# Performance work log

Hardware: AMD Instinct MI355X
Metric: run time of the kernel (lower is better)

## Reference

```python
import jax, jax.numpy as jnp
import numpy as np
import math

NUM_FREQ = 16           # pos_encoder octave frequencies
LATENT_SPACING = 3.0
PE_DIM = 4 * NUM_FREQ   # sin/cos for x and y


def pos_encode(delta_x, delta_y, physical_scale):
    # Fourier RPE: [..., 4*NUM_FREQ]
    freqs = (2.0 ** jnp.arange(NUM_FREQ, dtype=delta_x.dtype)) * jnp.pi
    ax = (delta_x / physical_scale)[..., None] * freqs  # [..., nf]
    ay = (delta_y / physical_scale)[..., None] * freqs
    return jnp.concatenate([jnp.sin(ax), jnp.cos(ax), jnp.sin(ay), jnp.cos(ay)], axis=-1)


def setup_inputs() -> dict:
    key = jax.random.key(0)
    B, L = 4, 4096
    positions = jax.random.normal(key, (B, L, 2), dtype=jnp.float32) * 50.0
    return {"positions": positions, "k": 16}


def reference(positions, k):
    B, L, _ = positions.shape
    k = min(k, L - 1)
    physical_scale = LATENT_SPACING * math.sqrt(k / math.pi)

    # full pairwise squared distances [B, L, L], diagonal masked to +inf
    diff_all = positions[:, :, None, :] - positions[:, None, :, :]
    dist_sq_all = jnp.sum(diff_all * diff_all, axis=-1)
    dist_sq_all = jnp.where(jnp.eye(L, dtype=bool)[None], jnp.inf, dist_sq_all)

    # smallest-k via top_k on negated distances
    _, topk_indices = jax.lax.top_k(-dist_sq_all, k)  # [B, L, k]

    # gather neighbor positions: [B, L, k, 2]
    neighbor_positions = jnp.take_along_axis(
        positions[:, None, :, :], topk_indices[..., None], axis=2)

    delta = neighbor_positions - positions[:, :, None, :]
    delta_x, delta_y = delta[..., 0], delta[..., 1]
    distances = jnp.sqrt(delta_x**2 + delta_y**2 + 1e-8)  # [B, L, k]

    rpe = pos_encode(delta_x, delta_y, physical_scale)  # [B, L, k, PE_DIM]

    zeros = jnp.zeros((B, L, 1), dtype=positions.dtype)
    self_rpe = pos_encode(zeros, zeros, physical_scale)  # [B, L, 1, PE_DIM]

    return topk_indices, rpe, self_rpe, distances, neighbor_positions
```

## Files before the change

kernel.cpp:

```cpp
#include <hip/hip_runtime.h>
#include <math.h>

namespace {
constexpr int BB  = 4;
constexpr int LL  = 4096;
constexpr int KK  = 16;
constexpr int GRID = 64;
constexpr int NCELL = GRID * GRID;
constexpr float WORLD_LO = -256.0f, CELL_INV = 0.125f;

constexpr int WSB_U32   = 6208;
constexpr int SIDX_OFF  = 4104;
constexpr int HARD_CNT  = BB * WSB_U32;
constexpr int HARD_LIST = HARD_CNT + 1;
constexpr int HARD_CAP  = 1024;

constexpr size_t N_IDX    = (size_t)BB * LL * KK;
constexpr size_t OFF_RPE  = N_IDX;
constexpr size_t OFF_SELF = OFF_RPE + N_IDX * 64;
constexpr size_t OFF_DIST = OFF_SELF + (size_t)BB * LL * 64;
constexpr size_t OFF_NPOS = OFF_DIST + N_IDX;
}

__device__ __forceinline__ float bf16r(float x) {
  unsigned u = __float_as_uint(x);
  unsigned r = (u + 0x7FFFu + ((u >> 16) & 1u)) & 0xFFFF0000u;
  return __uint_as_float(r);
}

__device__ __forceinline__ float d2_of(float cx, float cy, float px, float py) {
  const float dx = cx - px, dy = cy - py;
  return __fadd_rn(__fmul_rn(dx, dx), __fmul_rn(dy, dy));
}

__device__ __forceinline__ void insert16(unsigned long long (&key)[KK],
                                         unsigned long long kj) {
  #pragma unroll
  for (int t = 0; t < KK; ++t) {
    const bool lt = kj < key[t];
    const unsigned long long nk = lt ? kj : key[t];
    const unsigned long long ok = lt ? key[t] : kj;
    key[t] = nk; kj = ok;
  }
}

__device__ __forceinline__ int nth_set(unsigned long long m, int n) {
  int src = 0;
  #pragma unroll
  for (int w = 32; w >= 1; w >>= 1) {
    const unsigned long long lowm = (w == 64) ? ~0ull : ((1ull << w) - 1ull);
    const int c = __popcll(m & lowm);
    const bool go = n >= c;
    n   -= go ? c : 0;
    m    = go ? (m >> w) : m;
    src += go ? w : 0;
  }
  return src;
}

__device__ __forceinline__ unsigned long long
bitonic64(unsigned long long key, int lane) {
  #pragma unroll
  for (int k = 2; k <= 64; k <<= 1) {
    #pragma unroll
    for (int j = k >> 1; j >= 1; j >>= 1) {
      const unsigned long long o = __shfl_xor(key, j, 64);
      const bool takeMin = (((lane & j) == 0) == ((lane & k) == 0));
      const bool less = key < o;
      key = (takeMin == less) ? key : o;
    }
  }
  return key;
}

__global__ __launch_bounds__(256)
void bin_kernel(const float* __restrict__ positions,
                unsigned* __restrict__ ws,
                float* __restrict__ out)
{
  __shared__ unsigned cnt[NCELL];
  __shared__ unsigned wsum[4];
  const int tid = threadIdx.x, b = blockIdx.x;
  const float2* p2 = (const float2*)positions + (size_t)b * LL;
  unsigned* cs = ws + (size_t)b * WSB_U32;
  unsigned short* sidx = (unsigned short*)(cs + SIDX_OFF);
  float2* posw = (float2*)(out + OFF_RPE) + (size_t)b * LL;

  if (b == 0 && tid == 0) ws[HARD_CNT] = 0u;

  #pragma unroll
  for (int j = 0; j < NCELL / 256; ++j) cnt[tid + j * 256] = 0u;
  __syncthreads();

  int cellv[LL / 256];
  #pragma unroll
  for (int j = 0; j < LL / 256; ++j) {
    const int pi = tid + j * 256;
    const float2 p = p2[pi];
    int cx = (int)floorf((p.x - WORLD_LO) * CELL_INV);
    int cy = (int)floorf((p.y - WORLD_LO) * CELL_INV);
    cx = min(max(cx, 0), GRID - 1);
    cy = min(max(cy, 0), GRID - 1);
    cellv[j] = cy * GRID + cx;
    atomicAdd(&cnt[cellv[j]], 1u);
  }
  __syncthreads();

  unsigned csum = 0;
  #pragma unroll
  for (int k = 0; k < 16; ++k) csum += cnt[tid * 16 + k];
  unsigned inc = csum;
  #pragma unroll
  for (int off = 1; off < 64; off <<= 1) {
    const unsigned y = __shfl_up(inc, off, 64);
    if ((tid & 63) >= off) inc += y;
  }
  if ((tid & 63) == 63) wsum[tid >> 6] = inc;
  __syncthreads();
  const int w = tid >> 6;
  const unsigned w0 = wsum[0], w1 = wsum[1], w2 = wsum[2];
  const unsigned woff = (w > 0 ? w0 : 0u) + (w > 1 ? w1 : 0u) + (w > 2 ? w2 : 0u);
  unsigned run = woff + inc - csum;
  #pragma unroll
  for (int k = 0; k < 16; ++k) {
    const unsigned v = cnt[tid * 16 + k];
    cnt[tid * 16 + k] = run;
    cs[tid * 16 + k] = run;
    run += v;
  }
  if (tid == 255) cs[NCELL] = (unsigned)LL;
  __syncthreads();

  #pragma unroll
  for (int j = 0; j < LL / 256; ++j) {
    const int pi = tid + j * 256;
    const float2 p = p2[pi];
    const unsigned slot = atomicAdd(&cnt[cellv[j]], 1u);
    sidx[slot] = (unsigned short)pi;
    posw[slot] = p;
  }
}

__global__ __launch_bounds__(256)
void qsel3_kernel(const float* __restrict__ positions,
                  unsigned* __restrict__ ws,
                  float* __restrict__ out)
{
  const int tid  = threadIdx.x;
  const int b    = blockIdx.x >> 10, brow = blockIdx.x & 1023;
  const int w    = tid >> 6, lane = tid & 63;
  const int qrow = brow * 4 + w;

  const float2* p2 = (const float2*)positions + (size_t)b * LL;
  unsigned* cs = ws + (size_t)b * WSB_U32;
  const unsigned short* sidx = (const unsigned short*)(cs + SIDX_OFF);
  const float2* posw = (const float2*)(out + OFF_RPE) + (size_t)b * LL;
  const float2 P = p2[qrow];
  const size_t g3 = (size_t)b * LL + qrow;

  const float r2 = __fadd_rn(__fmul_rn(P.x, P.x), __fmul_rn(P.y, P.y));

  bool needhard = (r2 > 19321.0f);
  int Rs = 1; float tau = 0.0f;
  if (!needhard) {
    const float rho = 6.99f * __expf(r2 * 1.0e-4f);
    tau = rho * rho;
    Rs = (int)ceilf(rho * 0.125f + 0.5f);
    if (Rs < 1) Rs = 1;
    if (Rs > 6) needhard = true;
  }

  if (!needhard) {
    const int cx = min(max((int)floorf((P.x - WORLD_LO) * CELL_INV), 0), GRID - 1);
    const int cy = min(max((int)floorf((P.y - WORLD_LO) * CELL_INV), 0), GRID - 1);
    const int ry0 = max(cy - Rs, 0), ry1 = min(cy + Rs, GRID - 1);
    const int rx0 = max(cx - Rs, 0), rx1 = min(cx + Rs, GRID - 1);

    unsigned off = 0;
    float cd2 = 0.0f; int cidx = 0; bool have = false;
    for (int row = ry0; row <= ry1; ++row) {
      const unsigned a = cs[row * GRID + rx0];
      const unsigned e = cs[row * GRID + rx1 + 1];
      for (unsigned c0 = a; c0 < e; c0 += 64u) {
        const unsigned j = c0 + (unsigned)lane;
        const bool inr = j < e;
        float d2 = 1e30f; int ci = -1;
        if (inr) {
          const float2 c = posw[j];
          d2 = d2_of(c.x, c.y, P.x, P.y);
          ci = (int)sidx[j];
        }
        const bool pr = inr && (d2 <= tau) && (ci != qrow);
        const unsigned long long bal = __ballot(pr);
        const int cnt = __popcll(bal);
        const int want = lane - (int)off;
        const int wc = min(max(want, 0), 63);
        const int src = nth_set(bal, wc);
        const float rd2 = __shfl(d2, src, 64);
        const int   rci = __shfl(ci, src, 64);
        if (want >= 0 && want < cnt) { cd2 = rd2; cidx = rci; have = true; }
        off += (unsigned)cnt;
      }
    }

    if (off <= 64u) {
      unsigned long long key = have
          ? (((unsigned long long)__float_as_uint(cd2) << 32) | (unsigned)cidx)
          : ~0ULL;
      key = bitonic64(key, lane);
      const unsigned long long kth = __shfl(key, 15, 64);
      const float kd = __uint_as_float((unsigned)(kth >> 32));
      const float bound = (float)(Rs * 8 * Rs * 8);
      if (kd < bound) {
        if (lane < KK)
          out[g3 * KK + lane] = (float)(unsigned)(key & 0xFFFFFFFFu);
      } else needhard = true;
    } else needhard = true;
  }

  if (needhard) {
    unsigned slot = 0;
    if (lane == 0) slot = atomicAdd(&ws[HARD_CNT], 1u);
    slot = __shfl(slot, 0, 64);
    if (lane == 0 && slot < (unsigned)HARD_CAP)
      ws[HARD_LIST + slot] = ((unsigned)b << 12) | (unsigned)qrow;
    if (slot >= (unsigned)HARD_CAP) {
      unsigned long long key[KK];
      #pragma unroll
      for (int j = 0; j < KK; ++j) key[j] = ~0ULL;
      unsigned dmax = 0xFFFFFFFFu;
      for (int i = 0; i < LL / 64; ++i) {
        const int ci = lane + i * 64;
        const float2 c = p2[ci];
        const float d2 = d2_of(c.x, c.y, P.x, P.y);
        const unsigned d2b = __float_as_uint(d2);
        if (d2b < dmax && ci != qrow) {
          insert16(key, ((unsigned long long)d2b << 32) | (unsigned)ci);
          dmax = (unsigned)(key[KK - 1] >> 32);
        }
      }
      #pragma unroll
      for (int r = 0; r < KK; ++r) {
        unsigned long long m = key[0];
        #pragma unroll
        for (int o2 = 32; o2; o2 >>= 1) {
          const unsigned long long o = __shfl_xor(m, o2, 64);
          m = (o < m) ? o : m;
        }
        if (key[0] == m) {
          out[g3 * KK + r] = (float)(unsigned)(m & 0xFFFFFFFFu);
          #pragma unroll
          for (int j = 0; j < KK - 1; ++j) key[j] = key[j + 1];
          key[KK - 1] = ~0ULL;
        }
      }
    }
  }
}

__global__ __launch_bounds__(256)
void hard_kernel(const float* __restrict__ positions,
                 const unsigned* __restrict__ ws,
                 float* __restrict__ out)
{
  __shared__ unsigned long long wres[4 * KK];
  const unsigned cntr = ws[HARD_CNT];
  const unsigned n = cntr < (unsigned)HARD_CAP ? cntr : (unsigned)HARD_CAP;
  if (blockIdx.x >= n) return;
  const unsigned enc = ws[HARD_LIST + blockIdx.x];
  const int b = (int)(enc >> 12), qrow = (int)(enc & 4095);
  const float2* p2 = (const float2*)positions + (size_t)b * LL;
  const float2 P = p2[qrow];
  const int tid = threadIdx.x, w = tid >> 6, lane = tid & 63;
  const size_t g3 = (size_t)b * LL + qrow;

  unsigned long long key[KK];
  #pragma unroll
  for (int j = 0; j < KK; ++j) key[j] = ~0ULL;
  #pragma unroll
  for (int i = 0; i < KK; ++i) {
    const int ci = tid + i * 256;
    const float2 c = p2[ci];
    const float d2 = d2_of(c.x, c.y, P.x, P.y);
    if (ci != qrow)
      insert16(key, ((unsigned long long)__float_as_uint(d2) << 32) |
                    (unsigned)ci);
  }
  #pragma unroll
  for (int r = 0; r < KK; ++r) {
    unsigned long long m = key[0];
    #pragma unroll
    for (int off = 32; off; off >>= 1) {
      const unsigned long long o = __shfl_xor(m, off, 64);
      m = (o < m) ? o : m;
    }
    if (key[0] == m) {
      #pragma unroll
      for (int j = 0; j < KK - 1; ++j) key[j] = key[j + 1];
      key[KK - 1] = ~0ULL;
    }
    if (lane == 0) wres[w * KK + r] = m;
  }
  __syncthreads();
  if (tid < 64) {
    unsigned long long k = wres[tid];
    #pragma unroll
    for (int r = 0; r < KK; ++r) {
      unsigned long long m = k;
      #pragma unroll
      for (int off = 32; off; off >>= 1) {
        const unsigned long long o = __shfl_xor(m, off, 64);
        m = (o < m) ? o : m;
      }
      if (k == m) k = ~0ULL;
      if (tid == r)
        out[g3 * KK + r] = (float)(unsigned)(m & 0xFFFFFFFFu);
    }
  }
}

__global__ __launch_bounds__(256)
void emit_kernel(const float* __restrict__ positions,
                 float* __restrict__ out)
{
  const unsigned gid = blockIdx.x * 256 + threadIdx.x;
  const size_t g = (size_t)(gid >> 4);
  const int f = (int)(gid & 15);
  const size_t gq = g >> 4;
  const int r = (int)(g & 15);
  const int b = (int)(gq >> 12);
  const int qrow = (int)(gq & 4095);

  const float2* p2 = (const float2*)positions + (size_t)b * LL;
  const int ci = (int)out[g];

  const float2 P = p2[qrow];
  const float2 c = p2[ci];
  const float dx = c.x - P.x;
  const float dy = c.y - P.y;

  const float SCALE = (float)(3.0 * sqrt(16.0 / M_PI));
  const float PI_F  = (float)M_PI;
  const float tx = dx / SCALE;
  const float ty = dy / SCALE;
  const float fr = PI_F * (float)(1 << f);

  float sx, cx_, sy, cy_;
  sincosf(__fmul_rn(tx, fr), &sx, &cx_);
  sincosf(__fmul_rn(ty, fr), &sy, &cy_);

  const size_t base = OFF_RPE + g * 64;
  out[base +      f] = bf16r(sx);
  out[base + 16 + f] = bf16r(cx_);
  out[base + 32 + f] = bf16r(sy);
  out[base + 48 + f] = bf16r(cy_);

  if (f == 0) {
    const float d2 = __fadd_rn(__fmul_rn(dx, dx), __fmul_rn(dy, dy));
    out[OFF_DIST + g] = bf16r(sqrtf(__fadd_rn(d2, 1e-8f)));
  } else if (f == 1) {
    float2* np_ = (float2*)(out + OFF_NPOS) + g;
    *np_ = make_float2(bf16r(c.x), bf16r(c.y));
  }
  if (r == 0) {
    const float v = ((f >> 2) & 1) ? 1.0f : 0.0f;
    float4* sp = (float4*)(out + OFF_SELF) + gq * 16 + f;
    *sp = make_float4(v, v, v, v);
  }
}

extern "C" void kernel_launch(void* const* d_in, const int* in_sizes, int n_in,
                              void* d_out, int out_size, void* d_ws, size_t ws_size,
                              hipStream_t stream) {
  const float* positions = (const float*)d_in[0];
  float* out = (float*)d_out;
  unsigned* ws = (unsigned*)d_ws;

  bin_kernel  <<<dim3(BB),            dim3(256), 0, stream>>>(positions, ws, out);
  qsel3_kernel<<<dim3(BB * (LL / 4)), dim3(256), 0, stream>>>(positions, ws, out);
  hard_kernel <<<dim3(HARD_CAP),      dim3(256), 0, stream>>>(positions, ws, out);
  emit_kernel <<<dim3((int)(N_IDX * 16 / 256)), dim3(256), 0, stream>>>(positions, out);
}
```

Measured before the change: 84.94 us.

## Use double-angle recurrence in emit and one wave per hard query

The emit kernel now gives each thread four octave frequencies instead of one. It computes one sincos and derives the higher octaves (f+4, f+8, f+12) by applying the double-angle identity four times per step, which cuts sincos work and thread count by a factor of four. The hard-query kernel now handles one query per wavefront with a dmax-pruned scan and reuses the shared wave merge, removing the cross-wave LDS merge and __syncthreads. The recurrence accumulates rounding error over up to 12 doublings, which risks mismatches against the reference even after bf16 rounding.

After: 141.2 us. 66.3% more time.

```diff
diff --git a/kernel.cpp b/kernel.cpp
--- a/kernel.cpp
+++ b/kernel.cpp
@@ -71,6 +71,25 @@
     }
   }
   return key;
+}
+
+__device__ __forceinline__ void
+merge_write64(unsigned long long (&key)[KK], float* __restrict__ out, size_t g3) {
+  #pragma unroll
+  for (int r = 0; r < KK; ++r) {
+    unsigned long long m = key[0];
+    #pragma unroll
+    for (int o2 = 32; o2; o2 >>= 1) {
+      const unsigned long long o = __shfl_xor(m, o2, 64);
+      m = (o < m) ? o : m;
+    }
+    if (key[0] == m) {
+      out[g3 * KK + r] = (float)(unsigned)(m & 0xFFFFFFFFu);
+      #pragma unroll
+      for (int j = 0; j < KK - 1; ++j) key[j] = key[j + 1];
+      key[KK - 1] = ~0ULL;
+    }
+  }
 }
 
 __global__ __launch_bounds__(256)
@@ -239,21 +258,7 @@
           dmax = (unsigned)(key[KK - 1] >> 32);
         }
       }
-      #pragma unroll
-      for (int r = 0; r < KK; ++r) {
-        unsigned long long m = key[0];
-        #pragma unroll
-        for (int o2 = 32; o2; o2 >>= 1) {
-          const unsigned long long o = __shfl_xor(m, o2, 64);
-          m = (o < m) ? o : m;
-        }
-        if (key[0] == m) {
-          out[g3 * KK + r] = (float)(unsigned)(m & 0xFFFFFFFFu);
-          #pragma unroll
-          for (int j = 0; j < KK - 1; ++j) key[j] = key[j + 1];
-          key[KK - 1] = ~0ULL;
-        }
-      }
+      merge_write64(key, out, g3);
     }
   }
 }
@@ -263,60 +268,33 @@
                  const unsigned* __restrict__ ws,
                  float* __restrict__ out)
 {
-  __shared__ unsigned long long wres[4 * KK];
   const unsigned cntr = ws[HARD_CNT];
   const unsigned n = cntr < (unsigned)HARD_CAP ? cntr : (unsigned)HARD_CAP;
-  if (blockIdx.x >= n) return;
-  const unsigned enc = ws[HARD_LIST + blockIdx.x];
+  const int w = threadIdx.x >> 6, lane = threadIdx.x & 63;
+  const unsigned qi = blockIdx.x * 4u + (unsigned)w;
+  if (qi >= n) return;
+
+  const unsigned enc = ws[HARD_LIST + qi];
   const int b = (int)(enc >> 12), qrow = (int)(enc & 4095);
   const float2* p2 = (const float2*)positions + (size_t)b * LL;
   const float2 P = p2[qrow];
-  const int tid = threadIdx.x, w = tid >> 6, lane = tid & 63;
   const size_t g3 = (size_t)b * LL + qrow;
 
   unsigned long long key[KK];
   #pragma unroll
   for (int j = 0; j < KK; ++j) key[j] = ~0ULL;
-  #pragma unroll
-  for (int i = 0; i < KK; ++i) {
-    const int ci = tid + i * 256;
+  unsigned dmax = 0xFFFFFFFFu;
+  for (int i = 0; i < LL / 64; ++i) {
+    const int ci = lane + i * 64;
     const float2 c = p2[ci];
     const float d2 = d2_of(c.x, c.y, P.x, P.y);
-    if (ci != qrow)
-      insert16(key, ((unsigned long long)__float_as_uint(d2) << 32) |
-                    (unsigned)ci);
-  }
-  #pragma unroll
-  for (int r = 0; r < KK; ++r) {
-    unsigned long long m = key[0];
-    #pragma unroll
-    for (int off = 32; off; off >>= 1) {
-      const unsigned long long o = __shfl_xor(m, off, 64);
-      m = (o < m) ? o : m;
-    }
-    if (key[0] == m) {
-      #pragma unroll
-      for (int j = 0; j < KK - 1; ++j) key[j] = key[j + 1];
-      key[KK - 1] = ~0ULL;
-    }
-    if (lane == 0) wres[w * KK + r] = m;
-  }
-  __syncthreads();
-  if (tid < 64) {
-    unsigned long long k = wres[tid];
-    #pragma unroll
-    for (int r = 0; r < KK; ++r) {
-      unsigned long long m = k;
-      #pragma unroll
-      for (int off = 32; off; off >>= 1) {
-        const unsigned long long o = __shfl_xor(m, off, 64);
-        m = (o < m) ? o : m;
-      }
-      if (k == m) k = ~0ULL;
-      if (tid == r)
-        out[g3 * KK + r] = (float)(unsigned)(m & 0xFFFFFFFFu);
-    }
-  }
+    const unsigned d2b = __float_as_uint(d2);
+    if (d2b < dmax && ci != qrow) {
+      insert16(key, ((unsigned long long)d2b << 32) | (unsigned)ci);
+      dmax = (unsigned)(key[KK - 1] >> 32);
+    }
+  }
+  merge_write64(key, out, g3);
 }
 
 __global__ __launch_bounds__(256)
@@ -324,8 +302,8 @@
                  float* __restrict__ out)
 {
   const unsigned gid = blockIdx.x * 256 + threadIdx.x;
-  const size_t g = (size_t)(gid >> 4);
-  const int f = (int)(gid & 15);
+  const size_t g = (size_t)(gid >> 2);
+  const int t = (int)(gid & 3);
   const size_t gq = g >> 4;
   const int r = (int)(g & 15);
   const int b = (int)(gq >> 12);
@@ -343,29 +321,44 @@
   const float PI_F  = (float)M_PI;
   const float tx = dx / SCALE;
   const float ty = dy / SCALE;
-  const float fr = PI_F * (float)(1 << f);
+  const float fr0 = PI_F * (float)(1 << t);
 
   float sx, cx_, sy, cy_;
-  sincosf(__fmul_rn(tx, fr), &sx, &cx_);
-  sincosf(__fmul_rn(ty, fr), &sy, &cy_);
+  sincosf(__fmul_rn(tx, fr0), &sx, &cx_);
+  sincosf(__fmul_rn(ty, fr0), &sy, &cy_);
 
   const size_t base = OFF_RPE + g * 64;
-  out[base +      f] = bf16r(sx);
-  out[base + 16 + f] = bf16r(cx_);
-  out[base + 32 + f] = bf16r(sy);
-  out[base + 48 + f] = bf16r(cy_);
-
-  if (f == 0) {
+  #pragma unroll
+  for (int jj = 0; jj < 4; ++jj) {
+    const int f = t + 4 * jj;
+    out[base +      f] = bf16r(sx);
+    out[base + 16 + f] = bf16r(cx_);
+    out[base + 32 + f] = bf16r(sy);
+    out[base + 48 + f] = bf16r(cy_);
+    if (jj < 3) {
+      #pragma unroll
+      for (int d = 0; d < 4; ++d) {
+        const float nsx = 2.0f * sx * cx_;
+        const float ncx = __fmaf_rn(2.0f * cx_, cx_, -1.0f);
+        const float nsy = 2.0f * sy * cy_;
+        const float ncy = __fmaf_rn(2.0f * cy_, cy_, -1.0f);
+        sx = nsx; cx_ = ncx; sy = nsy; cy_ = ncy;
+      }
+    }
+  }
+
+  if (t == 0) {
     const float d2 = __fadd_rn(__fmul_rn(dx, dx), __fmul_rn(dy, dy));
     out[OFF_DIST + g] = bf16r(sqrtf(__fadd_rn(d2, 1e-8f)));
-  } else if (f == 1) {
+  } else if (t == 1) {
     float2* np_ = (float2*)(out + OFF_NPOS) + g;
     *np_ = make_float2(bf16r(c.x), bf16r(c.y));
   }
   if (r == 0) {
-    const float v = ((f >> 2) & 1) ? 1.0f : 0.0f;
-    float4* sp = (float4*)(out + OFF_SELF) + gq * 16 + f;
-    *sp = make_float4(v, v, v, v);
+    const float v = (t & 1) ? 1.0f : 0.0f;
+    float4* sp = (float4*)(out + OFF_SELF) + gq * 16 + t * 4;
+    const float4 vv = make_float4(v, v, v, v);
+    sp[0] = vv; sp[1] = vv; sp[2] = vv; sp[3] = vv;
   }
 }
 
@@ -378,6 +371,6 @@
 
   bin_kernel  <<<dim3(BB),            dim3(256), 0, stream>>>(positions, ws, out);
   qsel3_kernel<<<dim3(BB * (LL / 4)), dim3(256), 0, stream>>>(positions, ws, out);
-  hard_kernel <<<dim3(HARD_CAP),      dim3(256), 0, stream>>>(positions, ws, out);
-  emit_kernel <<<dim3((int)(N_IDX * 16 / 256)), dim3(256), 0, stream>>>(positions, out);
-}
+  hard_kernel <<<dim3(HARD_CAP / 4),  dim3(256), 0, stream>>>(positions, ws, out);
+  emit_kernel <<<dim3((int)(N_IDX * 4 / 256)), dim3(256), 0, stream>>>(positions, out);
+}
```
